# Kernel tuning notes

Hardware: AMD Instinct MI355X
Metric: run time of the kernel (lower is better)

Reference implementation:

```python
import jax, jax.numpy as jnp
import numpy as np

N, H, E, T, ED, AB = 50000, 64, 800000, 800000, 64, 16


def setup_inputs() -> dict:
    key = jax.random.key(0)
    ks = jax.random.split(key, 26)

    def nrm(k, shape, scale=1.0):
        return jax.random.normal(k, shape, dtype=jnp.float32) * scale

    d = {}
    d["s"] = nrm(ks[0], (N, H))
    d["v"] = nrm(ks[1], (N, H, 3))
    d["edge_index"] = jax.random.randint(ks[2], (2, E), 0, N, dtype=jnp.int32)
    d["edge_rbf"] = jax.random.uniform(ks[3], (E, ED), dtype=jnp.float32)
    raw_dir = jax.random.normal(ks[4], (E, 3), dtype=jnp.float32)
    d["edge_dir"] = raw_dir / jnp.linalg.norm(raw_dir, axis=-1, keepdims=True)
    d["triplet_kj"] = jax.random.randint(ks[5], (T,), 0, E, dtype=jnp.int32)
    d["triplet_ji"] = jax.random.randint(ks[6], (T,), 0, E, dtype=jnp.int32)
    d["angle_feat"] = jax.random.uniform(ks[7], (T, AB), dtype=jnp.float32)

    def lin(kw, kb, fan_in, fan_out):
        sc = 1.0 / np.sqrt(fan_in)
        return nrm(kw, (fan_in, fan_out), sc), nrm(kb, (fan_out,), sc)

    d["W_t1"], d["b_t1"] = lin(ks[8], ks[9], 2 * ED + AB, H)
    d["W_t2"], d["b_t2"] = lin(ks[10], ks[11], H, H)
    d["W_m1"], d["b_m1"] = lin(ks[12], ks[13], 2 * H + ED + H, H)
    d["W_m2"], d["b_m2"] = lin(ks[14], ks[15], H, 2 * H)
    d["W_u1"], d["b_u1"] = lin(ks[16], ks[17], 3 * H, H)
    d["W_u2"], d["b_u2"] = lin(ks[18], ks[19], H, H)
    d["W_g1"], d["b_g1"] = lin(ks[20], ks[21], 3 * H, H)
    d["W_g2"], d["b_g2"] = lin(ks[22], ks[23], H, H)
    d["ln_g"] = jnp.ones((H,), jnp.float32)
    d["ln_b"] = jnp.zeros((H,), jnp.float32)
    return d


def _mlp(x, W1, b1, W2, b2):
    return jax.nn.silu(x @ W1 + b1) @ W2 + b2


def reference(s, v, edge_index, edge_rbf, edge_dir, triplet_kj, triplet_ji,
              angle_feat, W_t1, b_t1, W_t2, b_t2, W_m1, b_m1, W_m2, b_m2,
              W_u1, b_u1, W_u2, b_u2, W_g1, b_g1, W_g2, b_g2, ln_g, ln_b):
    n_nodes, hid = s.shape
    n_edges = edge_rbf.shape[0]

    # 3-body triplet messages: gather two edge rbf rows + angle feature
    t_in = jnp.concatenate([edge_rbf[triplet_kj], edge_rbf[triplet_ji], angle_feat], axis=-1)
    t_msg = _mlp(t_in, W_t1, b_t1, W_t2, b_t2)                 # [T, H]
    angle_agg = jax.ops.segment_sum(t_msg, triplet_ji, num_segments=n_edges)  # [E, H]

    src, dst = edge_index[0], edge_index[1]
    msg_in = jnp.concatenate([s[src], s[dst], edge_rbf, angle_agg], axis=-1)  # [E, 4H]
    msg = _mlp(msg_in, W_m1, b_m1, W_m2, b_m2)                 # [E, 2H]
    m_s, m_v_coeff = jnp.split(msg, 2, axis=-1)

    agg_s = jax.ops.segment_sum(m_s, dst, num_segments=n_nodes)  # [N, H]
    m_v = m_v_coeff[:, :, None] * edge_dir[:, None, :]          # [E, H, 3]
    agg_v = jax.ops.segment_sum(m_v.reshape(n_edges, hid * 3), dst,
                                num_segments=n_nodes).reshape(n_nodes, hid, 3)

    v_norm = jnp.linalg.norm(v, axis=-1)                        # [N, H]
    ctx = jnp.concatenate([s, agg_s, v_norm], axis=-1)          # [N, 3H]
    s_new = s + _mlp(ctx, W_u1, b_u1, W_u2, b_u2)
    gate = jax.nn.sigmoid(_mlp(ctx, W_g1, b_g1, W_g2, b_g2))
    v_new = v + gate[..., None] * agg_v

    mu = s_new.mean(axis=-1, keepdims=True)
    var = s_new.var(axis=-1, keepdims=True)
    s_ln = (s_new - mu) / jnp.sqrt(var + 1e-5) * ln_g + ln_b
    s_out = jax.nn.silu(s_ln)
    return (s_out, v_new)
```

## Files before the change

### kernel.cpp

```cpp
#include <hip/hip_runtime.h>
#include <cstdint>
#include <cstddef>

#define NN 50000
#define NE 800000
#define NT 800000

typedef unsigned short u16;
typedef unsigned int u32;
typedef __attribute__((ext_vector_type(8))) short short8;
typedef __attribute__((ext_vector_type(4))) float f32x4;

__device__ __forceinline__ float silu_f(float x) { return x / (1.f + __expf(-x)); }
__device__ __forceinline__ float sigm_f(float x) { return 1.f / (1.f + __expf(-x)); }
__device__ __forceinline__ u16 f2b(float x) {
  u32 u = __float_as_uint(x);
  u32 r = u + 0x7fffu + ((u >> 16) & 1u);
  return (u16)(r >> 16);
}
__device__ __forceinline__ float b2f(u16 h) { return __uint_as_float(((u32)h) << 16); }

template <int RW>
__device__ __forceinline__ int lx(int r, int c) {
  return r * RW + ((((c >> 3) ^ (r & 7)) << 3) | (c & 7));
}

__global__ __launch_bounds__(256) void kcvt(const float* __restrict__ in,
                                            u16* __restrict__ out, int n4) {
  int i = blockIdx.x * 256 + threadIdx.x;
  if (i >= n4) return;
  float4 v = ((const float4*)in)[i];
  uint2 p;
  p.x = (u32)f2b(v.x) | ((u32)f2b(v.y) << 16);
  p.y = (u32)f2b(v.z) | ((u32)f2b(v.w) << 16);
  ((uint2*)out)[i] = p;
}

__global__ __launch_bounds__(256) void khist(const int* __restrict__ keys, int n,
                                             int* __restrict__ cnt) {
  int i = blockIdx.x * 256 + threadIdx.x;
  if (i < n) atomicAdd(&cnt[keys[i]], 1);
}

__global__ __launch_bounds__(256) void kscan1(const int* __restrict__ in, int n,
                                              int* __restrict__ out, int* __restrict__ bsum) {
  __shared__ int sh[256];
  int tid = threadIdx.x;
  size_t base = (size_t)blockIdx.x * 1024;
  int v[4];
  int acc = 0;
#pragma unroll
  for (int q = 0; q < 4; ++q) {
    size_t i = base + (size_t)tid * 4 + q;
    int x = (i < (size_t)n) ? in[i] : 0;
    v[q] = acc;
    acc += x;
  }
  sh[tid] = acc;
  __syncthreads();
  for (int off = 1; off < 256; off <<= 1) {
    int y = (tid >= off) ? sh[tid - off] : 0;
    __syncthreads();
    sh[tid] += y;
    __syncthreads();
  }
  int excl = (tid == 0) ? 0 : sh[tid - 1];
  if (tid == 255) bsum[blockIdx.x] = sh[255];
#pragma unroll
  for (int q = 0; q < 4; ++q) {
    size_t i = base + (size_t)tid * 4 + q;
    if (i < (size_t)n) out[i] = excl + v[q];
  }
}

__global__ __launch_bounds__(1024) void kscan2(int* __restrict__ bsum, int nb) {
  __shared__ int sh[1024];
  int tid = threadIdx.x;
  sh[tid] = (tid < nb) ? bsum[tid] : 0;
  __syncthreads();
  for (int off = 1; off < 1024; off <<= 1) {
    int y = (tid >= off) ? sh[tid - off] : 0;
    __syncthreads();
    sh[tid] += y;
    __syncthreads();
  }
  if (tid < nb) bsum[tid] = (tid == 0) ? 0 : sh[tid - 1];
}

__global__ __launch_bounds__(256) void kscan3(int* __restrict__ out, const int* __restrict__ bsum,
                                              int n, int total) {
  int i = blockIdx.x * 256 + threadIdx.x;
  if (i < n) out[i] += bsum[i >> 10];
  else if (i == n) out[n] = total;
}

__global__ __launch_bounds__(256) void kscatter_inv_afeat(
    const int* __restrict__ keys, const int* __restrict__ off, int n,
    int* __restrict__ cnt, int* __restrict__ tids,
    const float* __restrict__ afeat, u16* __restrict__ afeat_s) {
  int i = blockIdx.x * 256 + threadIdx.x;
  if (i < n) {
    int k = keys[i];
    int slot = off[k] + (atomicSub(&cnt[k], 1) - 1);
    tids[slot] = i;
    const float4* src = (const float4*)(afeat + (size_t)i * 16);
    uint2* dst = (uint2*)(afeat_s + (size_t)slot * 16);
#pragma unroll
    for (int q = 0; q < 4; ++q) {
      float4 v = src[q];
      uint2 p;
      p.x = (u32)f2b(v.x) | ((u32)f2b(v.y) << 16);
      p.y = (u32)f2b(v.z) | ((u32)f2b(v.w) << 16);
      dst[q] = p;
    }
  }
}

__global__ __launch_bounds__(256) void kscatter_inv_dir(const int* __restrict__ keys,
                                                        const int* __restrict__ off, int n,
                                                        int* __restrict__ cnt, int* __restrict__ inv,
                                                        const float* __restrict__ dir,
                                                        float* __restrict__ dir_s) {
  int i = blockIdx.x * 256 + threadIdx.x;
  if (i < n) {
    int k = keys[i];
    int slot = off[k] + (atomicSub(&cnt[k], 1) - 1);
    inv[i] = slot;
    dir_s[(size_t)slot * 3 + 0] = dir[(size_t)i * 3 + 0];
    dir_s[(size_t)slot * 3 + 1] = dir[(size_t)i * 3 + 1];
    dir_s[(size_t)slot * 3 + 2] = dir[(size_t)i * 3 + 2];
  }
}

__global__ __launch_bounds__(256) void kprepw(const float* __restrict__ W, int K, int Kp, int N,
                                              u16* __restrict__ out) {
  int tid = blockIdx.x * 256 + threadIdx.x;
  int total = (Kp / 32) * (N / 16) * 64;
  if (tid >= total) return;
  int l = tid & 63;
  int f = tid >> 6;
  int nt = f % (N / 16);
  int kt = f / (N / 16);
  int k0 = kt * 32 + (l >> 4) * 8;
  int n = nt * 16 + (l & 15);
  u16 vals[8];
#pragma unroll
  for (int j = 0; j < 8; ++j) {
    int kk = k0 + j;
    vals[j] = (kk < K) ? f2b(W[(size_t)kk * N + n]) : (u16)0;
  }
  uint4* dst = (uint4*)(out + (size_t)f * 512 + l * 8);
  uint4 p;
  p.x = (u32)vals[0] | ((u32)vals[1] << 16);
  p.y = (u32)vals[2] | ((u32)vals[3] << 16);
  p.z = (u32)vals[4] | ((u32)vals[5] << 16);
  p.w = (u32)vals[6] | ((u32)vals[7] << 16);
  *dst = p;
}

__global__ __launch_bounds__(256) void ktrip_mfma(
    const int* __restrict__ tkj, const int* __restrict__ tji,
    const u16* __restrict__ erbf_bf, const u16* __restrict__ afeat_s,
    const int* __restrict__ tids,
    const u16* __restrict__ Wp1, const float* __restrict__ b1,
    const u16* __restrict__ Wp2, const float* __restrict__ b2,
    u16* __restrict__ tmsg_s) {
  __shared__ u16 Xs[64 * 192];
  __shared__ u16 Hs[64 * 64];
  const int tid = threadIdx.x;
  const int l = tid & 63;
  const int w = tid >> 6;
  const int st0 = blockIdx.x * 64;

#pragma unroll
  for (int it = 0; it < 4; ++it) {
    int idx = it * 256 + tid;
    int sel = idx >> 9, r = (idx >> 3) & 63, ch = idx & 7;
    int t = tids[st0 + r];
    int node = sel ? tji[t] : tkj[t];
    uint4 vv = *(const uint4*)&erbf_bf[(size_t)node * 64 + ch * 8];
    *(uint4*)&Xs[lx<192>(r, sel * 64 + ch * 8)] = vv;
  }
  {
    int r = tid >> 2, c = (tid & 3) * 4;
    uint2 p2 = *(const uint2*)&afeat_s[(size_t)(st0 + r) * 16 + c];
    *(uint2*)&Xs[lx<192>(r, 128 + c)] = p2;
  }
#pragma unroll
  for (int i = 0; i < 2; ++i) {
    int idx = i * 256 + tid;
    int r = idx >> 3, c = 144 + (idx & 7) * 2;
    *(u32*)&Xs[lx<192>(r, c)] = 0;
  }
  __syncthreads();

  f32x4 acc1[4];
  {
    float bias = b1[w * 16 + (l & 15)];
#pragma unroll
    for (int mt = 0; mt < 4; ++mt) acc1[mt] = (f32x4){bias, bias, bias, bias};
    for (int ks = 0; ks < 5; ++ks) {
      short8 bf = *(const short8*)(Wp1 + ((size_t)(ks * 4 + w) * 64 + l) * 8);
#pragma unroll
      for (int mt = 0; mt < 4; ++mt) {
        short8 af = *(const short8*)&Xs[lx<192>(mt * 16 + (l & 15), ks * 32 + ((l >> 4) << 3))];
        acc1[mt] = __builtin_amdgcn_mfma_f32_16x16x32_bf16(af, bf, acc1[mt], 0, 0, 0);
      }
    }
  }
#pragma unroll
  for (int mt = 0; mt < 4; ++mt)
#pragma unroll
    for (int q = 0; q < 4; ++q) {
      int r = mt * 16 + (l >> 4) * 4 + q;
      Hs[lx<64>(r, w * 16 + (l & 15))] = f2b(silu_f(acc1[mt][q]));
    }
  __syncthreads();

  f32x4 acc2[4];
  {
    float bias = b2[w * 16 + (l & 15)];
#pragma unroll
    for (int mt = 0; mt < 4; ++mt) acc2[mt] = (f32x4){bias, bias, bias, bias};
    for (int ks = 0; ks < 2; ++ks) {
      short8 bf = *(const short8*)(Wp2 + ((size_t)(ks * 4 + w) * 64 + l) * 8);
#pragma unroll
      for (int mt = 0; mt < 4; ++mt) {
        short8 af = *(const short8*)&Hs[lx<64>(mt * 16 + (l & 15), ks * 32 + ((l >> 4) << 3))];
        acc2[mt] = __builtin_amdgcn_mfma_f32_16x16x32_bf16(af, bf, acc2[mt], 0, 0, 0);
      }
    }
  }
  __syncthreads();
#pragma unroll
  for (int mt = 0; mt < 4; ++mt)
#pragma unroll
    for (int q = 0; q < 4; ++q) {
      int r = mt * 16 + (l >> 4) * 4 + q;
      Xs[lx<64>(r, w * 16 + (l & 15))] = f2b(acc2[mt][q]);
    }
  __syncthreads();
  for (int i = 0; i < 2; ++i) {
    int idx = i * 256 + tid;
    int r = idx >> 3, c0 = (idx & 7) << 3;
    uint4 val = *(const uint4*)&Xs[lx<64>(r, c0)];
    *(uint4*)(tmsg_s + (size_t)(st0 + r) * 64 + c0) = val;
  }
}

__global__ __launch_bounds__(256) void kmsg_mfma(
    const int* __restrict__ eidx, const u16* __restrict__ s_bf,
    const u16* __restrict__ erbf_bf,
    const int* __restrict__ toff, const u16* __restrict__ tmsg_s,
    const int* __restrict__ eslot,
    const u16* __restrict__ Wp1, const float* __restrict__ b1,
    const u16* __restrict__ Wp2, const float* __restrict__ b2,
    u16* __restrict__ msg_s) {
  __shared__ u16 Xs[64 * 256];
  __shared__ u16 Hs[64 * 64];
  const int tid = threadIdx.x;
  const int l = tid & 63;
  const int w = tid >> 6;
  const int e0 = blockIdx.x * 64;

#pragma unroll
  for (int i = 0; i < 2; ++i) {
    int idx = i * 256 + tid;
    int r = idx >> 3, c0 = (idx & 7) << 3;
    uint4 vv = *(const uint4*)&erbf_bf[(size_t)(e0 + r) * 64 + c0];
    *(uint4*)&Xs[lx<256>(r, 128 + c0)] = vv;
  }
#pragma unroll
  for (int it = 0; it < 4; ++it) {
    int idx = it * 256 + tid;
    int sel = idx >> 9, r = (idx >> 3) & 63, ch = idx & 7;
    int node = eidx[sel * NE + e0 + r];
    uint4 vv = *(const uint4*)&s_bf[(size_t)node * 64 + ch * 8];
    *(uint4*)&Xs[lx<256>(r, sel * 64 + ch * 8)] = vv;
  }
#pragma unroll
  for (int it = 0; it < 2; ++it) {
    int idx = it * 256 + tid;
    int r = idx >> 3, ch = idx & 7;
    int e = e0 + r;
    int r0 = toff[e], r1 = toff[e + 1];
    float a[8];
#pragma unroll
    for (int j = 0; j < 8; ++j) a[j] = 0.f;
    for (int ri = r0; ri < r1; ++ri) {
      uint4 pk = *(const uint4*)&tmsg_s[(size_t)ri * 64 + ch * 8];
      a[0] += b2f((u16)(pk.x & 0xffff)); a[1] += b2f((u16)(pk.x >> 16));
      a[2] += b2f((u16)(pk.y & 0xffff)); a[3] += b2f((u16)(pk.y >> 16));
      a[4] += b2f((u16)(pk.z & 0xffff)); a[5] += b2f((u16)(pk.z >> 16));
      a[6] += b2f((u16)(pk.w & 0xffff)); a[7] += b2f((u16)(pk.w >> 16));
    }
    uint4 p;
    p.x = (u32)f2b(a[0]) | ((u32)f2b(a[1]) << 16);
    p.y = (u32)f2b(a[2]) | ((u32)f2b(a[3]) << 16);
    p.z = (u32)f2b(a[4]) | ((u32)f2b(a[5]) << 16);
    p.w = (u32)f2b(a[6]) | ((u32)f2b(a[7]) << 16);
    *(uint4*)&Xs[lx<256>(r, 192 + ch * 8)] = p;
  }
  __syncthreads();

  f32x4 acc1[4];
  {
    float bias = b1[w * 16 + (l & 15)];
#pragma unroll
    for (int mt = 0; mt < 4; ++mt) acc1[mt] = (f32x4){bias, bias, bias, bias};
    for (int ks = 0; ks < 8; ++ks) {
      short8 bf = *(const short8*)(Wp1 + ((size_t)(ks * 4 + w) * 64 + l) * 8);
#pragma unroll
      for (int mt = 0; mt < 4; ++mt) {
        short8 af = *(const short8*)&Xs[lx<256>(mt * 16 + (l & 15), ks * 32 + ((l >> 4) << 3))];
        acc1[mt] = __builtin_amdgcn_mfma_f32_16x16x32_bf16(af, bf, acc1[mt], 0, 0, 0);
      }
    }
  }
#pragma unroll
  for (int mt = 0; mt < 4; ++mt)
#pragma unroll
    for (int q = 0; q < 4; ++q) {
      int r = mt * 16 + (l >> 4) * 4 + q;
      Hs[lx<64>(r, w * 16 + (l & 15))] = f2b(silu_f(acc1[mt][q]));
    }
  __syncthreads();

  f32x4 acc2[2][4];
#pragma unroll
  for (int pp = 0; pp < 2; ++pp) {
    int nt = w * 2 + pp;
    float bias = b2[nt * 16 + (l & 15)];
#pragma unroll
    for (int mt = 0; mt < 4; ++mt) acc2[pp][mt] = (f32x4){bias, bias, bias, bias};
    for (int ks = 0; ks < 2; ++ks) {
      short8 bf = *(const short8*)(Wp2 + ((size_t)(ks * 8 + nt) * 64 + l) * 8);
#pragma unroll
      for (int mt = 0; mt < 4; ++mt) {
        short8 af = *(const short8*)&Hs[lx<64>(mt * 16 + (l & 15), ks * 32 + ((l >> 4) << 3))];
        acc2[pp][mt] = __builtin_amdgcn_mfma_f32_16x16x32_bf16(af, bf, acc2[pp][mt], 0, 0, 0);
      }
    }
  }
  __syncthreads();
#pragma unroll
  for (int pp = 0; pp < 2; ++pp)
#pragma unroll
    for (int mt = 0; mt < 4; ++mt)
#pragma unroll
      for (int q = 0; q < 4; ++q) {
        int r = mt * 16 + (l >> 4) * 4 + q;
        Xs[lx<128>(r, (w * 2 + pp) * 16 + (l & 15))] = f2b(acc2[pp][mt][q]);
      }
  __syncthreads();
  for (int i = 0; i < 4; ++i) {
    int idx = i * 256 + tid;
    int r = idx >> 4, c0 = (idx & 15) << 3;
    int slot = eslot[e0 + r];
    uint4 val = *(const uint4*)&Xs[lx<128>(r, c0)];
    *(uint4*)(msg_s + (size_t)slot * 128 + c0) = val;
  }
}

__global__ __launch_bounds__(256) void kagg(
    const int* __restrict__ noff, const u16* __restrict__ msg_s,
    const float* __restrict__ dir_s,
    u16* __restrict__ aggs_bf, float* __restrict__ aggv) {
  const int lane = threadIdx.x & 63;
  const int wv = threadIdx.x >> 6;
  const int n = blockIdx.x * 4 + wv;
  if (n >= NN) return;
  const int r0 = noff[n], r1 = noff[n + 1];
  const int lrow = lane >> 4, lcol = lane & 15;
  const bool is_ms = (lcol < 8);

  float a[8];
  float v0[8], v1[8], v2[8];
#pragma unroll
  for (int j = 0; j < 8; ++j) { a[j] = 0.f; v0[j] = 0.f; v1[j] = 0.f; v2[j] = 0.f; }

  for (int r4 = r0; r4 < r1; r4 += 4) {
    int r = r4 + lrow;
    if (r < r1) {
      uint4 pk = *(const uint4*)&msg_s[(size_t)r * 128 + lcol * 8];
      float x[8];
      x[0] = b2f((u16)(pk.x & 0xffff)); x[1] = b2f((u16)(pk.x >> 16));
      x[2] = b2f((u16)(pk.y & 0xffff)); x[3] = b2f((u16)(pk.y >> 16));
      x[4] = b2f((u16)(pk.z & 0xffff)); x[5] = b2f((u16)(pk.z >> 16));
      x[6] = b2f((u16)(pk.w & 0xffff)); x[7] = b2f((u16)(pk.w >> 16));
      if (is_ms) {
#pragma unroll
        for (int j = 0; j < 8; ++j) a[j] += x[j];
      } else {
        float dx = dir_s[(size_t)r * 3 + 0];
        float dy = dir_s[(size_t)r * 3 + 1];
        float dz = dir_s[(size_t)r * 3 + 2];
#pragma unroll
        for (int j = 0; j < 8; ++j) {
          v0[j] += x[j] * dx; v1[j] += x[j] * dy; v2[j] += x[j] * dz;
        }
      }
    }
  }
#pragma unroll
  for (int j = 0; j < 8; ++j) {
    a[j] += __shfl_xor(a[j], 16);  a[j] += __shfl_xor(a[j], 32);
    v0[j] += __shfl_xor(v0[j], 16); v0[j] += __shfl_xor(v0[j], 32);
    v1[j] += __shfl_xor(v1[j], 16); v1[j] += __shfl_xor(v1[j], 32);
    v2[j] += __shfl_xor(v2[j], 16); v2[j] += __shfl_xor(v2[j], 32);
  }
  if (lrow == 0) {
    if (is_ms) {
      uint4 p;
      p.x = (u32)f2b(a[0]) | ((u32)f2b(a[1]) << 16);
      p.y = (u32)f2b(a[2]) | ((u32)f2b(a[3]) << 16);
      p.z = (u32)f2b(a[4]) | ((u32)f2b(a[5]) << 16);
      p.w = (u32)f2b(a[6]) | ((u32)f2b(a[7]) << 16);
      *(uint4*)&aggs_bf[(size_t)n * 64 + lcol * 8] = p;
    } else {
      int c0 = (lcol - 8) * 8;
      float* av = aggv + (size_t)n * 192 + (size_t)c0 * 3;
      float4 o0 = {v0[0], v1[0], v2[0], v0[1]};
      float4 o1 = {v1[1], v2[1], v0[2], v1[2]};
      float4 o2 = {v2[2], v0[3], v1[3], v2[3]};
      float4 o3 = {v0[4], v1[4], v2[4], v0[5]};
      float4 o4 = {v1[5], v2[5], v0[6], v1[6]};
      float4 o5 = {v2[6], v0[7], v1[7], v2[7]};
      float4* av4 = (float4*)av;
      av4[0] = o0; av4[1] = o1; av4[2] = o2; av4[3] = o3; av4[4] = o4; av4[5] = o5;
    }
  }
}

__global__ __launch_bounds__(256) void knode_mfma(
    const u16* __restrict__ s_bf, const float* __restrict__ v,
    const u16* __restrict__ aggs_bf, const float* __restrict__ aggv,
    const u16* __restrict__ WpU1, const float* __restrict__ bU1,
    const u16* __restrict__ WpU2, const float* __restrict__ bU2,
    const u16* __restrict__ WpG1, const float* __restrict__ bG1,
    const u16* __restrict__ WpG2, const float* __restrict__ bG2,
    const float* __restrict__ lng, const float* __restrict__ lnb,
    float* __restrict__ outs, float* __restrict__ outv) {
  __shared__ __align__(16) char smem[64 * 192 * 2 + 2 * 64 * 64 * 2];
  u16* Xs = (u16*)smem;
  u16* Hu = (u16*)(smem + 64 * 192 * 2);
  u16* Hg = Hu + 64 * 64;
  float* Fs = (float*)smem;

  const int tid = threadIdx.x;
  const int l = tid & 63;
  const int w = tid >> 6;
  const int n0 = blockIdx.x * 64;

  for (int i = 0; i < 2; ++i) {
    int idx = i * 256 + tid;
    int r = idx >> 3, c0 = (idx & 7) << 3;
    int nr = n0 + r; if (nr >= NN) nr = NN - 1;
    uint4 a = *(const uint4*)&s_bf[(size_t)nr * 64 + c0];
    *(uint4*)&Xs[lx<192>(r, c0)] = a;
    uint4 b = *(const uint4*)&aggs_bf[(size_t)nr * 64 + c0];
    *(uint4*)&Xs[lx<192>(r, 64 + c0)] = b;
  }
  for (int it = 0; it < 16; ++it) {
    int idx = it * 256 + tid;
    int r = idx >> 6, c = idx & 63;
    int nr = n0 + r; if (nr >= NN) nr = NN - 1;
    const float* vp = v + (size_t)nr * 192 + c * 3;
    float x = vp[0], y = vp[1], z = vp[2];
    Xs[lx<192>(r, 128 + c)] = f2b(sqrtf(x * x + y * y + z * z));
  }
  __syncthreads();

  f32x4 au[4], ag[4];
  {
    float biu = bU1[w * 16 + (l & 15)], big = bG1[w * 16 + (l & 15)];
#pragma unroll
    for (int mt = 0; mt < 4; ++mt) {
      au[mt] = (f32x4){biu, biu, biu, biu};
      ag[mt] = (f32x4){big, big, big, big};
    }
    for (int ks = 0; ks < 6; ++ks) {
      short8 bu = *(const short8*)(WpU1 + ((size_t)(ks * 4 + w) * 64 + l) * 8);
      short8 bg = *(const short8*)(WpG1 + ((size_t)(ks * 4 + w) * 64 + l) * 8);
#pragma unroll
      for (int mt = 0; mt < 4; ++mt) {
        short8 af = *(const short8*)&Xs[lx<192>(mt * 16 + (l & 15), ks * 32 + ((l >> 4) << 3))];
        au[mt] = __builtin_amdgcn_mfma_f32_16x16x32_bf16(af, bu, au[mt], 0, 0, 0);
        ag[mt] = __builtin_amdgcn_mfma_f32_16x16x32_bf16(af, bg, ag[mt], 0, 0, 0);
      }
    }
  }
#pragma unroll
  for (int mt = 0; mt < 4; ++mt)
#pragma unroll
    for (int q = 0; q < 4; ++q) {
      int r = mt * 16 + (l >> 4) * 4 + q;
      Hu[lx<64>(r, w * 16 + (l & 15))] = f2b(silu_f(au[mt][q]));
      Hg[lx<64>(r, w * 16 + (l & 15))] = f2b(silu_f(ag[mt][q]));
    }
  __syncthreads();

  f32x4 ou[4], og[4];
  {
    float biu = bU2[w * 16 + (l & 15)], big = bG2[w * 16 + (l & 15)];
#pragma unroll
    for (int mt = 0; mt < 4; ++mt) {
      ou[mt] = (f32x4){biu, biu, biu, biu};
      og[mt] = (f32x4){big, big, big, big};
    }
    for (int ks = 0; ks < 2; ++ks) {
      short8 bu = *(const short8*)(WpU2 + ((size_t)(ks * 4 + w) * 64 + l) * 8);
      short8 bg = *(const short8*)(WpG2 + ((size_t)(ks * 4 + w) * 64 + l) * 8);
#pragma unroll
      for (int mt = 0; mt < 4; ++mt) {
        short8 afu = *(const short8*)&Hu[lx<64>(mt * 16 + (l & 15), ks * 32 + ((l >> 4) << 3))];
        ou[mt] = __builtin_amdgcn_mfma_f32_16x16x32_bf16(afu, bu, ou[mt], 0, 0, 0);
        short8 afg = *(const short8*)&Hg[lx<64>(mt * 16 + (l & 15), ks * 32 + ((l >> 4) << 3))];
        og[mt] = __builtin_amdgcn_mfma_f32_16x16x32_bf16(afg, bg, og[mt], 0, 0, 0);
      }
    }
  }
#pragma unroll
  for (int mt = 0; mt < 4; ++mt)
#pragma unroll
    for (int q = 0; q < 4; ++q) {
      int r = mt * 16 + (l >> 4) * 4 + q;
      ou[mt][q] += b2f(Xs[lx<192>(r, w * 16 + (l & 15))]);
    }
  __syncthreads();

#pragma unroll
  for (int mt = 0; mt < 4; ++mt)
#pragma unroll
    for (int q = 0; q < 4; ++q) {
      int r = mt * 16 + (l >> 4) * 4 + q;
      Fs[r * 68 + w * 16 + (l & 15)] = ou[mt][q];
    }
  __syncthreads();
  {
    int r = tid >> 2, c0 = (tid & 3) * 16;
    float xv[16];
#pragma unroll
    for (int j4 = 0; j4 < 4; ++j4) {
      float4 t = *(const float4*)&Fs[r * 68 + c0 + j4 * 4];
      xv[j4 * 4 + 0] = t.x; xv[j4 * 4 + 1] = t.y;
      xv[j4 * 4 + 2] = t.z; xv[j4 * 4 + 3] = t.w;
    }
    float sm = 0.f, sq = 0.f;
#pragma unroll
    for (int j = 0; j < 16; ++j) { sm += xv[j]; sq += xv[j] * xv[j]; }
    sm += __shfl_xor(sm, 1); sq += __shfl_xor(sq, 1);
    sm += __shfl_xor(sm, 2); sq += __shfl_xor(sq, 2);
    float mu = sm * (1.f / 64.f);
    float var = sq * (1.f / 64.f) - mu * mu;
    float rstd = rsqrtf(var + 1e-5f);
    if (n0 + r < NN) {
      float* op = outs + (size_t)(n0 + r) * 64 + c0;
#pragma unroll
      for (int j4 = 0; j4 < 4; ++j4) {
        float4 o;
        float y0 = (xv[j4 * 4 + 0] - mu) * rstd * lng[c0 + j4 * 4 + 0] + lnb[c0 + j4 * 4 + 0];
        float y1 = (xv[j4 * 4 + 1] - mu) * rstd * lng[c0 + j4 * 4 + 1] + lnb[c0 + j4 * 4 + 1];
        float y2 = (xv[j4 * 4 + 2] - mu) * rstd * lng[c0 + j4 * 4 + 2] + lnb[c0 + j4 * 4 + 2];
        float y3 = (xv[j4 * 4 + 3] - mu) * rstd * lng[c0 + j4 * 4 + 3] + lnb[c0 + j4 * 4 + 3];
        o.x = silu_f(y0); o.y = silu_f(y1); o.z = silu_f(y2); o.w = silu_f(y3);
        *(float4*)(op + j4 * 4) = o;
      }
    }
  }
  __syncthreads();

#pragma unroll
  for (int mt = 0; mt < 4; ++mt)
#pragma unroll
    for (int q = 0; q < 4; ++q) {
      int r = mt * 16 + (l >> 4) * 4 + q;
      Fs[r * 68 + w * 16 + (l & 15)] = og[mt][q];
    }
  __syncthreads();
  {
    int r = tid >> 2, c0 = (tid & 3) * 16;
    int nr = n0 + r;
    if (nr < NN) {
      float gate[16];
#pragma unroll
      for (int j = 0; j < 16; ++j) gate[j] = sigm_f(Fs[r * 68 + c0 + j]);
      const float4* vp = (const float4*)(v + (size_t)nr * 192 + c0 * 3);
      const float4* ap = (const float4*)(aggv + (size_t)nr * 192 + c0 * 3);
      float4* op = (float4*)(outv + (size_t)nr * 192 + c0 * 3);
#pragma unroll
      for (int j4 = 0; j4 < 12; ++j4) {
        float4 vv = vp[j4], av = ap[j4], o;
        o.x = vv.x + gate[(j4 * 4 + 0) / 3] * av.x;
        o.y = vv.y + gate[(j4 * 4 + 1) / 3] * av.y;
        o.z = vv.z + gate[(j4 * 4 + 2) / 3] * av.z;
        o.w = vv.w + gate[(j4 * 4 + 3) / 3] * av.w;
        op[j4] = o;
      }
    }
  }
}

extern "C" void kernel_launch(void* const* d_in, const int* in_sizes, int n_in,
                              void* d_out, int out_size, void* d_ws, size_t ws_size,
                              hipStream_t stream) {
  const float* s     = (const float*)d_in[0];
  const float* v     = (const float*)d_in[1];
  const int*   eidx  = (const int*)d_in[2];
  const float* erbf  = (const float*)d_in[3];
  const float* edir  = (const float*)d_in[4];
  const int*   tkj   = (const int*)d_in[5];
  const int*   tji   = (const int*)d_in[6];
  const float* afeat = (const float*)d_in[7];
  const float* W_t1  = (const float*)d_in[8];
  const float* b_t1  = (const float*)d_in[9];
  const float* W_t2  = (const float*)d_in[10];
  const float* b_t2  = (const float*)d_in[11];
  const float* W_m1  = (const float*)d_in[12];
  const float* b_m1  = (const float*)d_in[13];
  const float* W_m2  = (const float*)d_in[14];
  const float* b_m2  = (const float*)d_in[15];
  const float* W_u1  = (const float*)d_in[16];
  const float* b_u1  = (const float*)d_in[17];
  const float* W_u2  = (const float*)d_in[18];
  const float* b_u2  = (const float*)d_in[19];
  const float* W_g1  = (const float*)d_in[20];
  const float* b_g1  = (const float*)d_in[21];
  const float* W_g2  = (const float*)d_in[22];
  const float* b_g2  = (const float*)d_in[23];
  const float* ln_g  = (const float*)d_in[24];
  const float* ln_b  = (const float*)d_in[25];

  char* w = (char*)d_ws;
  auto alloc = [&](size_t bytes) -> char* {
    char* p = w;
    w += (bytes + 255) & ~(size_t)255;
    return p;
  };
  int* toff  = (int*)alloc((size_t)(NE + 1) * 4);
  int* noff  = (int*)alloc((size_t)(NN + 1) * 4);
  int* tcnt  = (int*)alloc((size_t)NE * 4);
  int* ncnt  = (int*)alloc((size_t)NN * 4);
  int* tids  = (int*)alloc((size_t)NT * 4);
  int* eslot = (int*)alloc((size_t)NE * 4);
  int* bsum  = (int*)alloc(1024 * 4);
  float* dir_s = (float*)alloc((size_t)NE * 3 * 4);
  u16* msg_s  = (u16*)alloc((size_t)NE * 128 * 2);
  u16* tmsg_s = (u16*)alloc((size_t)NT * 64 * 2);
  u16* erbf_bf = (u16*)alloc((size_t)NE * 64 * 2);
  u16* s_bf    = (u16*)alloc((size_t)NN * 64 * 2);
  u16* Wp_t1 = (u16*)alloc((size_t)5 * 4 * 512 * 2);
  u16* Wp_t2 = (u16*)alloc((size_t)2 * 4 * 512 * 2);
  u16* Wp_m1 = (u16*)alloc((size_t)8 * 4 * 512 * 2);
  u16* Wp_m2 = (u16*)alloc((size_t)2 * 8 * 512 * 2);
  u16* Wp_u1 = (u16*)alloc((size_t)6 * 4 * 512 * 2);
  u16* Wp_u2 = (u16*)alloc((size_t)2 * 4 * 512 * 2);
  u16* Wp_g1 = (u16*)alloc((size_t)6 * 4 * 512 * 2);
  u16* Wp_g2 = (u16*)alloc((size_t)2 * 4 * 512 * 2);
  u16* afeat_s = msg_s;
  float* aggv = (float*)tmsg_s;
  u16* aggs_bf = tmsg_s + (size_t)NN * 384;

  hipMemsetAsync(tcnt, 0, (size_t)NE * 4, stream);
  hipMemsetAsync(ncnt, 0, (size_t)NN * 4, stream);

  kcvt<<<(NE * 16 + 255) / 256, 256, 0, stream>>>(erbf, erbf_bf, NE * 16);
  kcvt<<<(NN * 16 + 255) / 256, 256, 0, stream>>>(s, s_bf, NN * 16);

  khist<<<(NT + 255) / 256, 256, 0, stream>>>(tji, NT, tcnt);
  khist<<<(NE + 255) / 256, 256, 0, stream>>>(eidx + NE, NE, ncnt);

  kscan1<<<(NE + 1023) / 1024, 256, 0, stream>>>(tcnt, NE, toff, bsum);
  kscan2<<<1, 1024, 0, stream>>>(bsum, (NE + 1023) / 1024);
  kscan3<<<(NE + 1 + 255) / 256, 256, 0, stream>>>(toff, bsum, NE, NT);
  kscatter_inv_afeat<<<(NT + 255) / 256, 256, 0, stream>>>(tji, toff, NT, tcnt, tids,
                                                           afeat, afeat_s);

  kscan1<<<(NN + 1023) / 1024, 256, 0, stream>>>(ncnt, NN, noff, bsum);
  kscan2<<<1, 1024, 0, stream>>>(bsum, (NN + 1023) / 1024);
  kscan3<<<(NN + 1 + 255) / 256, 256, 0, stream>>>(noff, bsum, NN, NE);
  kscatter_inv_dir<<<(NE + 255) / 256, 256, 0, stream>>>(eidx + NE, noff, NE, ncnt, eslot,
                                                         edir, dir_s);

  kprepw<<<5, 256, 0, stream>>>(W_t1, 144, 160, 64, Wp_t1);
  kprepw<<<2, 256, 0, stream>>>(W_t2, 64, 64, 64, Wp_t2);
  kprepw<<<8, 256, 0, stream>>>(W_m1, 256, 256, 64, Wp_m1);
  kprepw<<<4, 256, 0, stream>>>(W_m2, 64, 64, 128, Wp_m2);
  kprepw<<<6, 256, 0, stream>>>(W_u1, 192, 192, 64, Wp_u1);
  kprepw<<<2, 256, 0, stream>>>(W_u2, 64, 64, 64, Wp_u2);
  kprepw<<<6, 256, 0, stream>>>(W_g1, 192, 192, 64, Wp_g1);
  kprepw<<<2, 256, 0, stream>>>(W_g2, 64, 64, 64, Wp_g2);

  ktrip_mfma<<<NT / 64, 256, 0, stream>>>(tkj, tji, erbf_bf, afeat_s, tids,
                                          Wp_t1, b_t1, Wp_t2, b_t2, tmsg_s);
  kmsg_mfma<<<NE / 64, 256, 0, stream>>>(eidx, s_bf, erbf_bf, toff, tmsg_s, eslot,
                                         Wp_m1, b_m1, Wp_m2, b_m2, msg_s);
  kagg<<<(NN + 3) / 4, 256, 0, stream>>>(noff, msg_s, dir_s, aggs_bf, aggv);

  float* out_s = (float*)d_out;
  float* out_v = out_s + (size_t)NN * 64;
  knode_mfma<<<(NN + 63) / 64, 256, 0, stream>>>(s_bf, v, aggs_bf, aggv,
                                                 Wp_u1, b_u1, Wp_u2, b_u2,
                                                 Wp_g1, b_g1, Wp_g2, b_g2,
                                                 ln_g, ln_b, out_s, out_v);
}
```

Measured before the change: 684.9 us.

## Batch preprocessing launches and process edges in dst-sorted order in message kernel

Merges paired conversion, histogram, scan and weight-prep kernels into single launches, cutting the number of small kernel launches and memsets. The message kernel now walks edges in destination-sorted slot order through a forward edge-id list. It gathers each edge's inputs indirectly and writes message rows contiguously instead of scattering them. This trades the coalesced reads of edge rbf and toff for gathers in exchange for coalesced output writes.

```diff
diff --git a/kernel.cpp b/kernel.cpp
--- a/kernel.cpp
+++ b/kernel.cpp
@@ -25,28 +25,44 @@
   return r * RW + ((((c >> 3) ^ (r & 7)) << 3) | (c & 7));
 }
 
-__global__ __launch_bounds__(256) void kcvt(const float* __restrict__ in,
-                                            u16* __restrict__ out, int n4) {
+__global__ __launch_bounds__(256) void kcvt2(const float* __restrict__ erbf,
+                                             u16* __restrict__ erbf_bf,
+                                             const float* __restrict__ s,
+                                             u16* __restrict__ s_bf) {
   int i = blockIdx.x * 256 + threadIdx.x;
-  if (i >= n4) return;
-  float4 v = ((const float4*)in)[i];
+  const float* in;
+  u16* out;
+  int j;
+  if (i < NE * 16) { in = erbf; out = erbf_bf; j = i; }
+  else { j = i - NE * 16; if (j >= NN * 16) return; in = s; out = s_bf; }
+  float4 v = ((const float4*)in)[j];
   uint2 p;
   p.x = (u32)f2b(v.x) | ((u32)f2b(v.y) << 16);
   p.y = (u32)f2b(v.z) | ((u32)f2b(v.w) << 16);
-  ((uint2*)out)[i] = p;
-}
-
-__global__ __launch_bounds__(256) void khist(const int* __restrict__ keys, int n,
-                                             int* __restrict__ cnt) {
+  ((uint2*)out)[j] = p;
+}
+
+__global__ __launch_bounds__(256) void khist2(const int* __restrict__ tji,
+                                              const int* __restrict__ edst,
+                                              int* __restrict__ tcnt,
+                                              int* __restrict__ ncnt) {
   int i = blockIdx.x * 256 + threadIdx.x;
-  if (i < n) atomicAdd(&cnt[keys[i]], 1);
-}
-
-__global__ __launch_bounds__(256) void kscan1(const int* __restrict__ in, int n,
-                                              int* __restrict__ out, int* __restrict__ bsum) {
+  if (i < NT) atomicAdd(&tcnt[tji[i]], 1);
+  else {
+    int j = i - NT;
+    if (j < NE) atomicAdd(&ncnt[edst[j]], 1);
+  }
+}
+
+__global__ __launch_bounds__(256) void kscan1b(
+    const int* __restrict__ inA, int nA, int* __restrict__ outA, int* __restrict__ bsA, int BA,
+    const int* __restrict__ inB, int nB, int* __restrict__ outB, int* __restrict__ bsB) {
   __shared__ int sh[256];
+  const int* in; int n; int* out; int* bs; int blk;
+  if ((int)blockIdx.x < BA) { in = inA; n = nA; out = outA; bs = bsA; blk = blockIdx.x; }
+  else { in = inB; n = nB; out = outB; bs = bsB; blk = blockIdx.x - BA; }
   int tid = threadIdx.x;
-  size_t base = (size_t)blockIdx.x * 1024;
+  size_t base = (size_t)blk * 1024;
   int v[4];
   int acc = 0;
 #pragma unroll
@@ -65,7 +81,7 @@
     __syncthreads();
   }
   int excl = (tid == 0) ? 0 : sh[tid - 1];
-  if (tid == 255) bsum[blockIdx.x] = sh[255];
+  if (tid == 255) bs[blk] = sh[255];
 #pragma unroll
   for (int q = 0; q < 4; ++q) {
     size_t i = base + (size_t)tid * 4 + q;
@@ -73,10 +89,13 @@
   }
 }
 
-__global__ __launch_bounds__(1024) void kscan2(int* __restrict__ bsum, int nb) {
+__global__ __launch_bounds__(1024) void kscan2b(int* __restrict__ bsA, int nbA,
+                                                int* __restrict__ bsB, int nbB) {
   __shared__ int sh[1024];
+  int* bs = (blockIdx.x == 0) ? bsA : bsB;
+  int nb = (blockIdx.x == 0) ? nbA : nbB;
   int tid = threadIdx.x;
-  sh[tid] = (tid < nb) ? bsum[tid] : 0;
+  sh[tid] = (tid < nb) ? bs[tid] : 0;
   __syncthreads();
   for (int off = 1; off < 1024; off <<= 1) {
     int y = (tid >= off) ? sh[tid - off] : 0;
@@ -84,14 +103,21 @@
     sh[tid] += y;
     __syncthreads();
   }
-  if (tid < nb) bsum[tid] = (tid == 0) ? 0 : sh[tid - 1];
-}
-
-__global__ __launch_bounds__(256) void kscan3(int* __restrict__ out, const int* __restrict__ bsum,
-                                              int n, int total) {
+  if (tid < nb) bs[tid] = (tid == 0) ? 0 : sh[tid - 1];
+}
+
+__global__ __launch_bounds__(256) void kscan3b(
+    int* __restrict__ outA, const int* __restrict__ bsA, int nA, int totalA,
+    int* __restrict__ outB, const int* __restrict__ bsB, int nB, int totalB) {
   int i = blockIdx.x * 256 + threadIdx.x;
-  if (i < n) out[i] += bsum[i >> 10];
-  else if (i == n) out[n] = total;
+  if (i <= nA) {
+    if (i < nA) outA[i] += bsA[i >> 10];
+    else outA[nA] = totalA;
+  } else {
+    int j = i - (nA + 1);
+    if (j < nB) outB[j] += bsB[j >> 10];
+    else if (j == nB) outB[nB] = totalB;
+  }
 }
 
 __global__ __launch_bounds__(256) void kscatter_inv_afeat(
@@ -116,31 +142,46 @@
   }
 }
 
-__global__ __launch_bounds__(256) void kscatter_inv_dir(const int* __restrict__ keys,
+__global__ __launch_bounds__(256) void kscatter_fwd_dir(const int* __restrict__ keys,
                                                         const int* __restrict__ off, int n,
-                                                        int* __restrict__ cnt, int* __restrict__ inv,
+                                                        int* __restrict__ cnt,
+                                                        int* __restrict__ eids,
                                                         const float* __restrict__ dir,
                                                         float* __restrict__ dir_s) {
   int i = blockIdx.x * 256 + threadIdx.x;
   if (i < n) {
     int k = keys[i];
     int slot = off[k] + (atomicSub(&cnt[k], 1) - 1);
-    inv[i] = slot;
+    eids[slot] = i;
     dir_s[(size_t)slot * 3 + 0] = dir[(size_t)i * 3 + 0];
     dir_s[(size_t)slot * 3 + 1] = dir[(size_t)i * 3 + 1];
     dir_s[(size_t)slot * 3 + 2] = dir[(size_t)i * 3 + 2];
   }
 }
 
-__global__ __launch_bounds__(256) void kprepw(const float* __restrict__ W, int K, int Kp, int N,
-                                              u16* __restrict__ out) {
-  int tid = blockIdx.x * 256 + threadIdx.x;
-  int total = (Kp / 32) * (N / 16) * 64;
-  if (tid >= total) return;
-  int l = tid & 63;
-  int f = tid >> 6;
-  int nt = f % (N / 16);
-  int kt = f / (N / 16);
+__global__ __launch_bounds__(256) void kprepw_all(
+    const float* __restrict__ Wt1, const float* __restrict__ Wt2,
+    const float* __restrict__ Wm1, const float* __restrict__ Wm2,
+    const float* __restrict__ Wu1, const float* __restrict__ Wu2,
+    const float* __restrict__ Wg1, const float* __restrict__ Wg2,
+    u16* __restrict__ Pt1, u16* __restrict__ Pt2,
+    u16* __restrict__ Pm1, u16* __restrict__ Pm2,
+    u16* __restrict__ Pu1, u16* __restrict__ Pu2,
+    u16* __restrict__ Pg1, u16* __restrict__ Pg2) {
+  int gid = blockIdx.x * 256 + threadIdx.x;
+  int f = gid >> 6, l = gid & 63;
+  const float* W; u16* out; int K, N, fl;
+  if (f < 20)       { W = Wt1; out = Pt1; K = 144; N = 64;  fl = f; }
+  else if (f < 28)  { W = Wt2; out = Pt2; K = 64;  N = 64;  fl = f - 20; }
+  else if (f < 60)  { W = Wm1; out = Pm1; K = 256; N = 64;  fl = f - 28; }
+  else if (f < 76)  { W = Wm2; out = Pm2; K = 64;  N = 128; fl = f - 60; }
+  else if (f < 100) { W = Wu1; out = Pu1; K = 192; N = 64;  fl = f - 76; }
+  else if (f < 108) { W = Wu2; out = Pu2; K = 64;  N = 64;  fl = f - 100; }
+  else if (f < 132) { W = Wg1; out = Pg1; K = 192; N = 64;  fl = f - 108; }
+  else if (f < 140) { W = Wg2; out = Pg2; K = 64;  N = 64;  fl = f - 132; }
+  else return;
+  int nt = fl % (N / 16);
+  int kt = fl / (N / 16);
   int k0 = kt * 32 + (l >> 4) * 8;
   int n = nt * 16 + (l & 15);
   u16 vals[8];
@@ -149,7 +190,7 @@
     int kk = k0 + j;
     vals[j] = (kk < K) ? f2b(W[(size_t)kk * N + n]) : (u16)0;
   }
-  uint4* dst = (uint4*)(out + (size_t)f * 512 + l * 8);
+  uint4* dst = (uint4*)(out + (size_t)fl * 512 + l * 8);
   uint4 p;
   p.x = (u32)vals[0] | ((u32)vals[1] << 16);
   p.y = (u32)vals[2] | ((u32)vals[3] << 16);
@@ -252,7 +293,7 @@
     const int* __restrict__ eidx, const u16* __restrict__ s_bf,
     const u16* __restrict__ erbf_bf,
     const int* __restrict__ toff, const u16* __restrict__ tmsg_s,
-    const int* __restrict__ eslot,
+    const int* __restrict__ eids,
     const u16* __restrict__ Wp1, const float* __restrict__ b1,
     const u16* __restrict__ Wp2, const float* __restrict__ b2,
     u16* __restrict__ msg_s) {
@@ -261,20 +302,22 @@
   const int tid = threadIdx.x;
   const int l = tid & 63;
   const int w = tid >> 6;
-  const int e0 = blockIdx.x * 64;
+  const int sl0 = blockIdx.x * 64;
 
 #pragma unroll
   for (int i = 0; i < 2; ++i) {
     int idx = i * 256 + tid;
     int r = idx >> 3, c0 = (idx & 7) << 3;
-    uint4 vv = *(const uint4*)&erbf_bf[(size_t)(e0 + r) * 64 + c0];
+    int e = eids[sl0 + r];
+    uint4 vv = *(const uint4*)&erbf_bf[(size_t)e * 64 + c0];
     *(uint4*)&Xs[lx<256>(r, 128 + c0)] = vv;
   }
 #pragma unroll
   for (int it = 0; it < 4; ++it) {
     int idx = it * 256 + tid;
     int sel = idx >> 9, r = (idx >> 3) & 63, ch = idx & 7;
-    int node = eidx[sel * NE + e0 + r];
+    int e = eids[sl0 + r];
+    int node = eidx[sel * NE + e];
     uint4 vv = *(const uint4*)&s_bf[(size_t)node * 64 + ch * 8];
     *(uint4*)&Xs[lx<256>(r, sel * 64 + ch * 8)] = vv;
   }
@@ -282,7 +325,7 @@
   for (int it = 0; it < 2; ++it) {
     int idx = it * 256 + tid;
     int r = idx >> 3, ch = idx & 7;
-    int e = e0 + r;
+    int e = eids[sl0 + r];
     int r0 = toff[e], r1 = toff[e + 1];
     float a[8];
 #pragma unroll
@@ -356,9 +399,8 @@
   for (int i = 0; i < 4; ++i) {
     int idx = i * 256 + tid;
     int r = idx >> 4, c0 = (idx & 15) << 3;
-    int slot = eslot[e0 + r];
     uint4 val = *(const uint4*)&Xs[lx<128>(r, c0)];
-    *(uint4*)(msg_s + (size_t)slot * 128 + c0) = val;
+    *(uint4*)(msg_s + (size_t)(sl0 + r) * 128 + c0) = val;
   }
 }
 
@@ -642,8 +684,8 @@
   int* tcnt  = (int*)alloc((size_t)NE * 4);
   int* ncnt  = (int*)alloc((size_t)NN * 4);
   int* tids  = (int*)alloc((size_t)NT * 4);
-  int* eslot = (int*)alloc((size_t)NE * 4);
-  int* bsum  = (int*)alloc(1024 * 4);
+  int* eids  = (int*)alloc((size_t)NE * 4);
+  int* bsum  = (int*)alloc(2048 * 4);
   float* dir_s = (float*)alloc((size_t)NE * 3 * 4);
   u16* msg_s  = (u16*)alloc((size_t)NE * 128 * 2);
   u16* tmsg_s = (u16*)alloc((size_t)NT * 64 * 2);
@@ -661,39 +703,28 @@
   float* aggv = (float*)tmsg_s;
   u16* aggs_bf = tmsg_s + (size_t)NN * 384;
 
-  hipMemsetAsync(tcnt, 0, (size_t)NE * 4, stream);
-  hipMemsetAsync(ncnt, 0, (size_t)NN * 4, stream);
-
-  kcvt<<<(NE * 16 + 255) / 256, 256, 0, stream>>>(erbf, erbf_bf, NE * 16);
-  kcvt<<<(NN * 16 + 255) / 256, 256, 0, stream>>>(s, s_bf, NN * 16);
-
-  khist<<<(NT + 255) / 256, 256, 0, stream>>>(tji, NT, tcnt);
-  khist<<<(NE + 255) / 256, 256, 0, stream>>>(eidx + NE, NE, ncnt);
-
-  kscan1<<<(NE + 1023) / 1024, 256, 0, stream>>>(tcnt, NE, toff, bsum);
-  kscan2<<<1, 1024, 0, stream>>>(bsum, (NE + 1023) / 1024);
-  kscan3<<<(NE + 1 + 255) / 256, 256, 0, stream>>>(toff, bsum, NE, NT);
+  hipMemsetAsync(tcnt, 0, (size_t)((char*)(ncnt + NN) - (char*)tcnt), stream);
+
+  kcvt2<<<(NE * 16 + NN * 16 + 255) / 256, 256, 0, stream>>>(erbf, erbf_bf, s, s_bf);
+  khist2<<<(NT + NE + 255) / 256, 256, 0, stream>>>(tji, eidx + NE, tcnt, ncnt);
+
+  const int Bt = (NE + 1023) / 1024, Bn = (NN + 1023) / 1024;
+  kscan1b<<<Bt + Bn, 256, 0, stream>>>(tcnt, NE, toff, bsum, Bt, ncnt, NN, noff, bsum + 1024);
+  kscan2b<<<2, 1024, 0, stream>>>(bsum, Bt, bsum + 1024, Bn);
+  kscan3b<<<(NE + 1 + NN + 1 + 255) / 256, 256, 0, stream>>>(toff, bsum, NE, NT,
+                                                             noff, bsum + 1024, NN, NE);
+
   kscatter_inv_afeat<<<(NT + 255) / 256, 256, 0, stream>>>(tji, toff, NT, tcnt, tids,
                                                            afeat, afeat_s);
-
-  kscan1<<<(NN + 1023) / 1024, 256, 0, stream>>>(ncnt, NN, noff, bsum);
-  kscan2<<<1, 1024, 0, stream>>>(bsum, (NN + 1023) / 1024);
-  kscan3<<<(NN + 1 + 255) / 256, 256, 0, stream>>>(noff, bsum, NN, NE);
-  kscatter_inv_dir<<<(NE + 255) / 256, 256, 0, stream>>>(eidx + NE, noff, NE, ncnt, eslot,
+  kscatter_fwd_dir<<<(NE + 255) / 256, 256, 0, stream>>>(eidx + NE, noff, NE, ncnt, eids,
                                                          edir, dir_s);
 
-  kprepw<<<5, 256, 0, stream>>>(W_t1, 144, 160, 64, Wp_t1);
-  kprepw<<<2, 256, 0, stream>>>(W_t2, 64, 64, 64, Wp_t2);
-  kprepw<<<8, 256, 0, stream>>>(W_m1, 256, 256, 64, Wp_m1);
-  kprepw<<<4, 256, 0, stream>>>(W_m2, 64, 64, 128, Wp_m2);
-  kprepw<<<6, 256, 0, stream>>>(W_u1, 192, 192, 64, Wp_u1);
-  kprepw<<<2, 256, 0, stream>>>(W_u2, 64, 64, 64, Wp_u2);
-  kprepw<<<6, 256, 0, stream>>>(W_g1, 192, 192, 64, Wp_g1);
-  kprepw<<<2, 256, 0, stream>>>(W_g2, 64, 64, 64, Wp_g2);
+  kprepw_all<<<35, 256, 0, stream>>>(W_t1, W_t2, W_m1, W_m2, W_u1, W_u2, W_g1, W_g2,
+                                     Wp_t1, Wp_t2, Wp_m1, Wp_m2, Wp_u1, Wp_u2, Wp_g1, Wp_g2);
 
   ktrip_mfma<<<NT / 64, 256, 0, stream>>>(tkj, tji, erbf_bf, afeat_s, tids,
                                           Wp_t1, b_t1, Wp_t2, b_t2, tmsg_s);
-  kmsg_mfma<<<NE / 64, 256, 0, stream>>>(eidx, s_bf, erbf_bf, toff, tmsg_s, eslot,
+  kmsg_mfma<<<NE / 64, 256, 0, stream>>>(eidx, s_bf, erbf_bf, toff, tmsg_s, eids,
                                          Wp_m1, b_m1, Wp_m2, b_m2, msg_s);
   kagg<<<(NN + 3) / 4, 256, 0, stream>>>(noff, msg_s, dir_s, aggs_bf, aggv);
 
```

New measurement: 643.5 us. 6.0% less time.
